# Performance work log

Hardware: AMD Instinct MI355X
Metric: run time of the kernel (lower is better)

Reference implementation:

```python
import jax, jax.numpy as jnp
import numpy as np

VIEW, SEQ, HID = 8, 2048, 1024
ATT = HID // VIEW  # 128


def setup_inputs() -> dict:
    key = jax.random.key(0)
    ks = jax.random.split(key, 12)
    std = 0.02
    return {
        "q": jax.random.normal(ks[0], (VIEW, SEQ, HID), jnp.float32),
        "k": jax.random.normal(ks[1], (VIEW, SEQ, HID), jnp.float32),
        "v": jax.random.normal(ks[2], (VIEW, SEQ, HID), jnp.float32),
        "attn_bias": jax.random.normal(ks[3], (VIEW, SEQ, SEQ), jnp.float32) * std,
        "wq": jax.random.normal(ks[4], (HID, ATT), jnp.float32) * std,
        "bq": jnp.zeros((ATT,), jnp.float32),
        "wk": jax.random.normal(ks[5], (HID, ATT), jnp.float32) * std,
        "bk": jnp.zeros((ATT,), jnp.float32),
        "wv": jax.random.normal(ks[6], (HID, ATT), jnp.float32) * std,
        "bv": jnp.zeros((ATT,), jnp.float32),
        "wo": jax.random.normal(ks[7], (VIEW * ATT, HID), jnp.float32) * std,
        "bo": jnp.zeros((HID,), jnp.float32),
    }


def reference(q, k, v, attn_bias, wq, bq, wk, bk, wv, bv, wo, bo):
    att = wq.shape[1]
    scale = att ** (-0.5)
    qh = (q @ wq + bq) * scale            # [V, S, A]
    kh = k @ wk + bk                      # [V, S, A]
    vh = v @ wv + bv                      # [V, S, A]
    scores = jnp.einsum("vqa,vka->vqk", qh, kh)   # [V, S, S]
    attn = jax.nn.softmax(scores, axis=2)
    # NOTE: source adds the bias AFTER softmax; dropout p=0 (identity).
    attn = attn + attn_bias
    x = jnp.einsum("vqk,vka->vqa", attn, vh)      # [V, S, A]
    vdim, sdim, adim = x.shape
    x = jnp.transpose(x, (1, 0, 2)).reshape(sdim, vdim * adim)  # [S, V*A]
    return x @ wo + bo                    # [S, HID]
```

## Files before the change

kernel.cpp:

```cpp
#include <hip/hip_runtime.h>
#include <math.h>

#define VIEWS 8
#define SEQ 2048
#define HID 1024
#define ATT 128
#define QSCALE 0.08838834764831845f

typedef __attribute__((ext_vector_type(8))) short short8;
typedef __attribute__((ext_vector_type(4))) float f32x4;

__device__ __forceinline__ unsigned short f2bf(float f) {
  union { float f; unsigned u; } a; a.f = f;
  unsigned r = a.u + 0x7FFF + ((a.u >> 16) & 1);
  return (unsigned short)(r >> 16);
}

__global__ __launch_bounds__(256)
void transpose_cvt_f32_bf16(const float* __restrict__ in,
                            unsigned short* __restrict__ out, int R, int C) {
  __shared__ alignas(16) unsigned short T[64][72];
  const int tid = threadIdx.x;
  const int r0 = blockIdx.y * 64, c0 = blockIdx.x * 64;
  const int tr = tid >> 2, tc = (tid & 3) * 16;
#pragma unroll
  for (int u = 0; u < 4; ++u) {
    float4 t = *(const float4*)&in[(size_t)(r0 + tr) * C + c0 + tc + u * 4];
    T[tc + u * 4 + 0][tr] = f2bf(t.x);
    T[tc + u * 4 + 1][tr] = f2bf(t.y);
    T[tc + u * 4 + 2][tr] = f2bf(t.z);
    T[tc + u * 4 + 3][tr] = f2bf(t.w);
  }
  __syncthreads();
  const int oc = tid >> 2, orr = (tid & 3) * 16;
#pragma unroll
  for (int u = 0; u < 2; ++u)
    *(short8*)&out[(size_t)(c0 + oc) * R + r0 + orr + u * 8] =
        *(const short8*)&T[oc][orr + u * 8];
}

__global__ __launch_bounds__(256)
void transpose_qkvw(const float* __restrict__ wq, const float* __restrict__ wk,
                    const float* __restrict__ wv, unsigned short* __restrict__ oq,
                    unsigned short* __restrict__ ok, unsigned short* __restrict__ ov) {
  __shared__ alignas(16) unsigned short T[64][72];
  const int z = blockIdx.z;
  const float* in = (z == 0) ? wq : (z == 1) ? wk : wv;
  unsigned short* out = (z == 0) ? oq : (z == 1) ? ok : ov;
  const int R = HID, C = ATT;
  const int tid = threadIdx.x;
  const int r0 = blockIdx.y * 64, c0 = blockIdx.x * 64;
  const int tr = tid >> 2, tc = (tid & 3) * 16;
#pragma unroll
  for (int u = 0; u < 4; ++u) {
    float4 t = *(const float4*)&in[(size_t)(r0 + tr) * C + c0 + tc + u * 4];
    T[tc + u * 4 + 0][tr] = f2bf(t.x);
    T[tc + u * 4 + 1][tr] = f2bf(t.y);
    T[tc + u * 4 + 2][tr] = f2bf(t.z);
    T[tc + u * 4 + 3][tr] = f2bf(t.w);
  }
  __syncthreads();
  const int oc = tid >> 2, orr = (tid & 3) * 16;
#pragma unroll
  for (int u = 0; u < 2; ++u)
    *(short8*)&out[(size_t)(c0 + oc) * R + r0 + orr + u * 8] =
        *(const short8*)&T[oc][orr + u * 8];
}

__global__ __launch_bounds__(256, 4)
void qkv_proj(const float* __restrict__ q, const float* __restrict__ k,
              const float* __restrict__ v, const unsigned short* __restrict__ wqT,
              const unsigned short* __restrict__ wkT,
              const unsigned short* __restrict__ wvT,
              const float* __restrict__ bq, const float* __restrict__ bk,
              const float* __restrict__ bv, unsigned short* __restrict__ qh,
              unsigned short* __restrict__ kh, unsigned short* __restrict__ vhT) {
  const int z = blockIdx.z;
  const float* A = (z == 0) ? q : (z == 1) ? k : v;
  const unsigned short* B = (z == 0) ? wqT : (z == 1) ? wkT : wvT;
  const float* bias = (z == 0) ? bq : (z == 1) ? bk : bv;
  const float scale = (z == 0) ? QSCALE : 1.0f;
  const int tid = threadIdx.x;
  const int w = tid >> 6, lane = tid & 63;
  const int l16 = lane & 15, quad = lane >> 4;
  const int mbase = blockIdx.x * 32 + (w & 1) * 16;
  const int n0 = (w >> 1) * 64;

  const float* arow = &A[(size_t)(mbase + l16) * HID + quad * 8];
  const unsigned short* bbase = &B[(size_t)(n0 + l16) * HID + quad * 8];

  f32x4 acc[4];
#pragma unroll
  for (int i = 0; i < 4; ++i) acc[i] = (f32x4)0.f;

#pragma unroll 2
  for (int k0 = 0; k0 < HID; k0 += 64) {
    const float4 a0 = *(const float4*)&arow[k0];
    const float4 a1 = *(const float4*)&arow[k0 + 4];
    const float4 a2 = *(const float4*)&arow[k0 + 32];
    const float4 a3 = *(const float4*)&arow[k0 + 36];
    short8 bfr[8];
#pragma unroll
    for (int nt = 0; nt < 4; ++nt) {
      bfr[nt * 2]     = *(const short8*)&bbase[(size_t)nt * 16 * HID + k0];
      bfr[nt * 2 + 1] = *(const short8*)&bbase[(size_t)nt * 16 * HID + k0 + 32];
    }
    short8 af0, af1;
    af0[0] = (short)f2bf(a0.x); af0[1] = (short)f2bf(a0.y);
    af0[2] = (short)f2bf(a0.z); af0[3] = (short)f2bf(a0.w);
    af0[4] = (short)f2bf(a1.x); af0[5] = (short)f2bf(a1.y);
    af0[6] = (short)f2bf(a1.z); af0[7] = (short)f2bf(a1.w);
    af1[0] = (short)f2bf(a2.x); af1[1] = (short)f2bf(a2.y);
    af1[2] = (short)f2bf(a2.z); af1[3] = (short)f2bf(a2.w);
    af1[4] = (short)f2bf(a3.x); af1[5] = (short)f2bf(a3.y);
    af1[6] = (short)f2bf(a3.z); af1[7] = (short)f2bf(a3.w);
#pragma unroll
    for (int nt = 0; nt < 4; ++nt) {
      acc[nt] = __builtin_amdgcn_mfma_f32_16x16x32_bf16(af0, bfr[nt * 2],     acc[nt], 0, 0, 0);
      acc[nt] = __builtin_amdgcn_mfma_f32_16x16x32_bf16(af1, bfr[nt * 2 + 1], acc[nt], 0, 0, 0);
    }
  }

  if (z < 2) {
    unsigned short* outp = (z == 0) ? qh : kh;
#pragma unroll
    for (int nt = 0; nt < 4; ++nt) {
      const int col = n0 + nt * 16 + l16;
      const float bvv = bias[col];
#pragma unroll
      for (int reg = 0; reg < 4; ++reg) {
        const int row = mbase + quad * 4 + reg;
        outp[(size_t)row * ATT + col] = f2bf((acc[nt][reg] + bvv) * scale);
      }
    }
  } else {
    const int gr = mbase + quad * 4;
    const int vi = gr >> 11, s = gr & (SEQ - 1);
#pragma unroll
    for (int nt = 0; nt < 4; ++nt) {
      const int col = n0 + nt * 16 + l16;
      const float bvv = bias[col];
      ushort4 pk;
      pk.x = f2bf(acc[nt][0] + bvv);
      pk.y = f2bf(acc[nt][1] + bvv);
      pk.z = f2bf(acc[nt][2] + bvv);
      pk.w = f2bf(acc[nt][3] + bvv);
      *(ushort4*)&vhT[((size_t)vi * ATT + col) * SEQ + s] = pk;
    }
  }
}

__global__ __launch_bounds__(256, 1)
void flash_fused(const unsigned short* __restrict__ qh,
                 const unsigned short* __restrict__ kh,
                 const unsigned short* __restrict__ vhT,
                 const float* __restrict__ ab,
                 unsigned short* __restrict__ xbf) {
  __shared__ alignas(16) unsigned short Qs[64][136];
  __shared__ alignas(16) unsigned short Ks[2][64][136];
  __shared__ alignas(16) unsigned short VTs[2][128][72];
  __shared__ alignas(16) unsigned short Ps[64][72];
  const int tid = threadIdx.x;
  const int vi = blockIdx.x;
  const int q0 = blockIdx.y * 64;
  const int w = tid >> 6, lane = tid & 63;
  const int l16 = lane & 15, quad = lane >> 4;
  const int wb = w * 16;

  const int kr_ = tid >> 2, kc_ = (tid & 3) * 32;
  const int vr_ = tid >> 1, vc_ = (tid & 1) * 32;
  const unsigned short* kbase = &kh[((size_t)vi * SEQ + kr_) * ATT + kc_];
  const unsigned short* vbase = &vhT[((size_t)vi * ATT + vr_) * SEQ + vc_];

  {
    const int r = tid >> 2, c = (tid & 3) * 32;
    const unsigned short* src = &qh[((size_t)vi * SEQ + q0 + r) * ATT + c];
#pragma unroll
    for (int u = 0; u < 4; ++u)
      *(short8*)&Qs[r][c + u * 8] = *(const short8*)&src[u * 8];
  }

  short8 krg[4], vrg[4];
#pragma unroll
  for (int u = 0; u < 4; ++u) krg[u] = *(const short8*)&kbase[u * 8];
#pragma unroll
  for (int u = 0; u < 4; ++u) vrg[u] = *(const short8*)&vbase[u * 8];

  __syncthreads();
  short8 aF[4];
#pragma unroll
  for (int ks = 0; ks < 4; ++ks)
    aF[ks] = *(const short8*)&Qs[wb + l16][ks * 32 + quad * 8];

  float l_r[4] = {0.f, 0.f, 0.f, 0.f};
  f32x4 o[8], o2[8];
#pragma unroll
  for (int i = 0; i < 8; ++i) { o[i] = (f32x4)0.f; o2[i] = (f32x4)0.f; }

  const float* abrow = &ab[((size_t)vi * SEQ + q0 + wb + l16) * SEQ];

  for (int t = 0; t < SEQ / 64; ++t) {
    const int kt = t * 64;
    const int cur = t & 1;
    float4 abv[4];
    abv[0] = *(const float4*)&abrow[kt + quad * 8];
    abv[1] = *(const float4*)&abrow[kt + quad * 8 + 4];
    abv[2] = *(const float4*)&abrow[kt + 32 + quad * 8];
    abv[3] = *(const float4*)&abrow[kt + 32 + quad * 8 + 4];
#pragma unroll
    for (int u = 0; u < 4; ++u)
      *(short8*)&Ks[cur][kr_][kc_ + u * 8] = krg[u];
#pragma unroll
    for (int u = 0; u < 4; ++u)
      *(short8*)&VTs[cur][vr_][vc_ + u * 8] = vrg[u];
    __syncthreads();
    if (t + 1 < SEQ / 64) {
      const unsigned short* kp = kbase + (size_t)(kt + 64) * ATT;
      const unsigned short* vp = vbase + (kt + 64);
#pragma unroll
      for (int u = 0; u < 4; ++u) krg[u] = *(const short8*)&kp[u * 8];
#pragma unroll
      for (int u = 0; u < 4; ++u) vrg[u] = *(const short8*)&vp[u * 8];
    }
    f32x4 sc[4];
#pragma unroll
    for (int i = 0; i < 4; ++i) sc[i] = (f32x4)0.f;
#pragma unroll
    for (int nt = 0; nt < 4; ++nt) {
#pragma unroll
      for (int ks = 0; ks < 4; ++ks) {
        short8 bF = *(const short8*)&Ks[cur][nt * 16 + l16][ks * 32 + quad * 8];
        sc[nt] = __builtin_amdgcn_mfma_f32_16x16x32_bf16(aF[ks], bF, sc[nt], 0, 0, 0);
      }
    }
#pragma unroll
    for (int nt = 0; nt < 4; ++nt) {
#pragma unroll
      for (int reg = 0; reg < 4; ++reg) {
        float p = __expf(sc[nt][reg]);
        l_r[reg] += p;
        Ps[wb + quad * 4 + reg][nt * 16 + l16] = f2bf(p);
      }
    }
#pragma unroll
    for (int ks = 0; ks < 2; ++ks) {
      short8 pF = *(const short8*)&Ps[wb + l16][ks * 32 + quad * 8];
      short8 bB;
      {
        const float4 u0 = abv[ks * 2], u1 = abv[ks * 2 + 1];
        bB[0] = (short)f2bf(u0.x); bB[1] = (short)f2bf(u0.y);
        bB[2] = (short)f2bf(u0.z); bB[3] = (short)f2bf(u0.w);
        bB[4] = (short)f2bf(u1.x); bB[5] = (short)f2bf(u1.y);
        bB[6] = (short)f2bf(u1.z); bB[7] = (short)f2bf(u1.w);
      }
#pragma unroll
      for (int at = 0; at < 8; ++at) {
        short8 vF = *(const short8*)&VTs[cur][at * 16 + l16][ks * 32 + quad * 8];
        o[at]  = __builtin_amdgcn_mfma_f32_16x16x32_bf16(pF, vF, o[at], 0, 0, 0);
        o2[at] = __builtin_amdgcn_mfma_f32_16x16x32_bf16(bB, vF, o2[at], 0, 0, 0);
      }
    }
  }
  float inv_l[4];
#pragma unroll
  for (int reg = 0; reg < 4; ++reg) {
    float l = l_r[reg];
    l += __shfl_xor(l, 1, 64);
    l += __shfl_xor(l, 2, 64);
    l += __shfl_xor(l, 4, 64);
    l += __shfl_xor(l, 8, 64);
    inv_l[reg] = 1.0f / l;
  }
#pragma unroll
  for (int at = 0; at < 8; ++at) {
    const int col = vi * ATT + at * 16 + l16;
#pragma unroll
    for (int reg = 0; reg < 4; ++reg) {
      const int row = q0 + wb + quad * 4 + reg;
      xbf[(size_t)row * HID + col] = f2bf(o[at][reg] * inv_l[reg] + o2[at][reg]);
    }
  }
}

__global__ __launch_bounds__(256)
void outproj_gemm(const unsigned short* __restrict__ A,
                  const unsigned short* __restrict__ B,
                  const float* __restrict__ bias, float* __restrict__ out) {
  __shared__ alignas(16) unsigned short As[2][64][72];
  __shared__ alignas(16) unsigned short Bs[2][128][72];
  const int tid = threadIdx.x;
  const int m0 = blockIdx.x * 64;
  const int n0 = blockIdx.y * 128;
  const int w = tid >> 6, lane = tid & 63;
  const int l16 = lane & 15, quad = lane >> 4;
  const int ar = tid >> 2, ac = (tid & 3) * 16;
  const int br = tid >> 1, bc = (tid & 1) * 32;
  const unsigned short* abase = &A[(size_t)(m0 + ar) * HID + ac];
  const unsigned short* bbase = &B[(size_t)(n0 + br) * HID + bc];

  f32x4 acc[8];
#pragma unroll
  for (int i = 0; i < 8; ++i) acc[i] = (f32x4)0.f;

  short8 arg0, arg1, brg[4];
  arg0 = *(const short8*)&abase[0];
  arg1 = *(const short8*)&abase[8];
#pragma unroll
  for (int u = 0; u < 4; ++u) brg[u] = *(const short8*)&bbase[u * 8];

  for (int kk = 0; kk < HID / 64; ++kk) {
    const int cur = kk & 1;
    *(short8*)&As[cur][ar][ac]     = arg0;
    *(short8*)&As[cur][ar][ac + 8] = arg1;
#pragma unroll
    for (int u = 0; u < 4; ++u)
      *(short8*)&Bs[cur][br][bc + u * 8] = brg[u];
    __syncthreads();
    if (kk + 1 < HID / 64) {
      const unsigned short* ap = abase + (kk + 1) * 64;
      const unsigned short* bp = bbase + (kk + 1) * 64;
      arg0 = *(const short8*)&ap[0];
      arg1 = *(const short8*)&ap[8];
#pragma unroll
      for (int u = 0; u < 4; ++u) brg[u] = *(const short8*)&bp[u * 8];
    }
#pragma unroll
    for (int ks = 0; ks < 2; ++ks) {
      short8 af = *(const short8*)&As[cur][w * 16 + l16][ks * 32 + quad * 8];
#pragma unroll
      for (int nt = 0; nt < 8; ++nt) {
        short8 bf = *(const short8*)&Bs[cur][nt * 16 + l16][ks * 32 + quad * 8];
        acc[nt] = __builtin_amdgcn_mfma_f32_16x16x32_bf16(af, bf, acc[nt], 0, 0, 0);
      }
    }
  }
#pragma unroll
  for (int nt = 0; nt < 8; ++nt) {
    const int col = n0 + nt * 16 + l16;
    const float bvv = bias[col];
#pragma unroll
    for (int reg = 0; reg < 4; ++reg) {
      const int row = m0 + w * 16 + quad * 4 + reg;
      out[(size_t)row * HID + col] = acc[nt][reg] + bvv;
    }
  }
}

extern "C" void kernel_launch(void* const* d_in, const int* in_sizes, int n_in,
                              void* d_out, int out_size, void* d_ws, size_t ws_size,
                              hipStream_t stream) {
  const float* q   = (const float*)d_in[0];
  const float* k   = (const float*)d_in[1];
  const float* v   = (const float*)d_in[2];
  const float* ab  = (const float*)d_in[3];
  const float* wq  = (const float*)d_in[4];
  const float* bq  = (const float*)d_in[5];
  const float* wk  = (const float*)d_in[6];
  const float* bk  = (const float*)d_in[7];
  const float* wv  = (const float*)d_in[8];
  const float* bv  = (const float*)d_in[9];
  const float* wo  = (const float*)d_in[10];
  const float* bo  = (const float*)d_in[11];
  float* out = (float*)d_out;

  char* ws = (char*)d_ws;
  const size_t PROJ_B = (size_t)VIEWS * SEQ * ATT * 2;
  unsigned short* qh  = (unsigned short*)(ws);
  unsigned short* kh  = (unsigned short*)(ws + PROJ_B);
  unsigned short* vhT = (unsigned short*)(ws + 2 * PROJ_B);
  unsigned short* xbf = (unsigned short*)(ws + 3 * PROJ_B);
  char* wbase = ws + 4 * PROJ_B;
  unsigned short* wqT = (unsigned short*)(wbase);
  unsigned short* wkT = (unsigned short*)(wbase + 262144);
  unsigned short* wvT = (unsigned short*)(wbase + 2 * 262144);
  unsigned short* woT = (unsigned short*)(wbase + 3 * 262144);

  dim3 blk(256);
  transpose_qkvw<<<dim3(2, 16, 3), blk, 0, stream>>>(wq, wk, wv, wqT, wkT, wvT);
  transpose_cvt_f32_bf16<<<dim3(16, 16), blk, 0, stream>>>(wo, woT, HID, HID);
  qkv_proj<<<dim3(512, 1, 3), blk, 0, stream>>>(q, k, v, wqT, wkT, wvT,
                                                bq, bk, bv, qh, kh, vhT);
  flash_fused<<<dim3(VIEWS, SEQ / 64), blk, 0, stream>>>(qh, kh, vhT, ab, xbf);
  outproj_gemm<<<dim3(SEQ / 64, HID / 128), blk, 0, stream>>>(xbf, woT, bo, out);
}
```

Baseline: 486.0 us.

## Stage QKV projection operands via LDS async loads and halve flash query tile

```diff
diff --git a/kernel.cpp b/kernel.cpp
--- a/kernel.cpp
+++ b/kernel.cpp
@@ -9,6 +9,11 @@
 
 typedef __attribute__((ext_vector_type(8))) short short8;
 typedef __attribute__((ext_vector_type(4))) float f32x4;
+
+#define GLOAD_LDS16(g, l)                                                     \
+  __builtin_amdgcn_global_load_lds(                                           \
+      (const __attribute__((address_space(1))) unsigned int*)(g),             \
+      (__attribute__((address_space(3))) unsigned int*)(l), 16, 0, 0)
 
 __device__ __forceinline__ unsigned short f2bf(float f) {
   union { float f; unsigned u; } a; a.f = f;
@@ -67,7 +72,7 @@
         *(const short8*)&T[oc][orr + u * 8];
 }
 
-__global__ __launch_bounds__(256, 4)
+__global__ __launch_bounds__(256, 2)
 void qkv_proj(const float* __restrict__ q, const float* __restrict__ k,
               const float* __restrict__ v, const unsigned short* __restrict__ wqT,
               const unsigned short* __restrict__ wkT,
@@ -75,6 +80,8 @@
               const float* __restrict__ bq, const float* __restrict__ bk,
               const float* __restrict__ bv, unsigned short* __restrict__ qh,
               unsigned short* __restrict__ kh, unsigned short* __restrict__ vhT) {
+  __shared__ alignas(16) float Af[2][32][64];
+  __shared__ alignas(16) unsigned short Bf[2][128][64];
   const int z = blockIdx.z;
   const float* A = (z == 0) ? q : (z == 1) ? k : v;
   const unsigned short* B = (z == 0) ? wqT : (z == 1) ? wkT : wvT;
@@ -83,28 +90,40 @@
   const int tid = threadIdx.x;
   const int w = tid >> 6, lane = tid & 63;
   const int l16 = lane & 15, quad = lane >> 4;
-  const int mbase = blockIdx.x * 32 + (w & 1) * 16;
+  const int m0 = blockIdx.x * 32;
+  const int wm = (w & 1) * 16;
   const int n0 = (w >> 1) * 64;
 
-  const float* arow = &A[(size_t)(mbase + l16) * HID + quad * 8];
-  const unsigned short* bbase = &B[(size_t)(n0 + l16) * HID + quad * 8];
+  const float* ag[2];
+#pragma unroll
+  for (int j = 0; j < 2; ++j)
+    ag[j] = &A[(size_t)(m0 + (w * 2 + j) * 4 + (lane >> 4)) * HID + (lane & 15) * 4];
+  const unsigned short* bg[4];
+#pragma unroll
+  for (int j = 0; j < 4; ++j)
+    bg[j] = &B[(size_t)((w * 4 + j) * 8 + (lane >> 3)) * HID + (lane & 7) * 8];
 
   f32x4 acc[4];
 #pragma unroll
   for (int i = 0; i < 4; ++i) acc[i] = (f32x4)0.f;
 
-#pragma unroll 2
-  for (int k0 = 0; k0 < HID; k0 += 64) {
-    const float4 a0 = *(const float4*)&arow[k0];
-    const float4 a1 = *(const float4*)&arow[k0 + 4];
-    const float4 a2 = *(const float4*)&arow[k0 + 32];
-    const float4 a3 = *(const float4*)&arow[k0 + 36];
-    short8 bfr[8];
-#pragma unroll
-    for (int nt = 0; nt < 4; ++nt) {
-      bfr[nt * 2]     = *(const short8*)&bbase[(size_t)nt * 16 * HID + k0];
-      bfr[nt * 2 + 1] = *(const short8*)&bbase[(size_t)nt * 16 * HID + k0 + 32];
-    }
+#define QKV_STAGE(nxt, k0)                                                    \
+  do {                                                                        \
+    _Pragma("unroll") for (int j = 0; j < 2; ++j)                             \
+        GLOAD_LDS16(ag[j] + (k0), &Af[nxt][(w * 2 + j) * 4][0]);              \
+    _Pragma("unroll") for (int j = 0; j < 4; ++j)                             \
+        GLOAD_LDS16(bg[j] + (k0), &Bf[nxt][(w * 4 + j) * 8][0]);              \
+  } while (0)
+
+  QKV_STAGE(0, 0);
+  int cur = 0;
+  for (int kk = 0; kk < HID / 64; ++kk) {
+    __syncthreads();
+    if (kk + 1 < HID / 64) QKV_STAGE(cur ^ 1, (kk + 1) * 64);
+    const float4 a0 = *(const float4*)&Af[cur][wm + l16][quad * 8];
+    const float4 a1 = *(const float4*)&Af[cur][wm + l16][quad * 8 + 4];
+    const float4 a2 = *(const float4*)&Af[cur][wm + l16][32 + quad * 8];
+    const float4 a3 = *(const float4*)&Af[cur][wm + l16][36 + quad * 8];
     short8 af0, af1;
     af0[0] = (short)f2bf(a0.x); af0[1] = (short)f2bf(a0.y);
     af0[2] = (short)f2bf(a0.z); af0[3] = (short)f2bf(a0.w);
@@ -116,10 +135,14 @@
     af1[6] = (short)f2bf(a3.z); af1[7] = (short)f2bf(a3.w);
 #pragma unroll
     for (int nt = 0; nt < 4; ++nt) {
-      acc[nt] = __builtin_amdgcn_mfma_f32_16x16x32_bf16(af0, bfr[nt * 2],     acc[nt], 0, 0, 0);
-      acc[nt] = __builtin_amdgcn_mfma_f32_16x16x32_bf16(af1, bfr[nt * 2 + 1], acc[nt], 0, 0, 0);
-    }
-  }
+      const short8 b0 = *(const short8*)&Bf[cur][n0 + nt * 16 + l16][quad * 8];
+      const short8 b1 = *(const short8*)&Bf[cur][n0 + nt * 16 + l16][32 + quad * 8];
+      acc[nt] = __builtin_amdgcn_mfma_f32_16x16x32_bf16(af0, b0, acc[nt], 0, 0, 0);
+      acc[nt] = __builtin_amdgcn_mfma_f32_16x16x32_bf16(af1, b1, acc[nt], 0, 0, 0);
+    }
+    cur ^= 1;
+  }
+#undef QKV_STAGE
 
   if (z < 2) {
     unsigned short* outp = (z == 0) ? qh : kh;
@@ -129,12 +152,12 @@
       const float bvv = bias[col];
 #pragma unroll
       for (int reg = 0; reg < 4; ++reg) {
-        const int row = mbase + quad * 4 + reg;
+        const int row = m0 + wm + quad * 4 + reg;
         outp[(size_t)row * ATT + col] = f2bf((acc[nt][reg] + bvv) * scale);
       }
     }
   } else {
-    const int gr = mbase + quad * 4;
+    const int gr = m0 + wm + quad * 4;
     const int vi = gr >> 11, s = gr & (SEQ - 1);
 #pragma unroll
     for (int nt = 0; nt < 4; ++nt) {
@@ -150,22 +173,25 @@
   }
 }
 
-__global__ __launch_bounds__(256, 1)
+__global__ __launch_bounds__(256, 2)
 void flash_fused(const unsigned short* __restrict__ qh,
                  const unsigned short* __restrict__ kh,
                  const unsigned short* __restrict__ vhT,
                  const float* __restrict__ ab,
                  unsigned short* __restrict__ xbf) {
-  __shared__ alignas(16) unsigned short Qs[64][136];
+  __shared__ alignas(16) char QPs[32 * 136 * 2];
   __shared__ alignas(16) unsigned short Ks[2][64][136];
   __shared__ alignas(16) unsigned short VTs[2][128][72];
-  __shared__ alignas(16) unsigned short Ps[64][72];
+  unsigned short (*Qs)[136] = (unsigned short(*)[136])QPs;
+  unsigned short (*Ps)[72]  = (unsigned short(*)[72])QPs;
+  float* Ls = (float*)(QPs + 32 * 72 * 2);
   const int tid = threadIdx.x;
   const int vi = blockIdx.x;
-  const int q0 = blockIdx.y * 64;
+  const int q0 = blockIdx.y * 32;
   const int w = tid >> 6, lane = tid & 63;
   const int l16 = lane & 15, quad = lane >> 4;
-  const int wb = w * 16;
+  const int wq_ = (w & 1) * 16;
+  const int wh = w >> 1;
 
   const int kr_ = tid >> 2, kc_ = (tid & 3) * 32;
   const int vr_ = tid >> 1, vc_ = (tid & 1) * 32;
@@ -173,13 +199,11 @@
   const unsigned short* vbase = &vhT[((size_t)vi * ATT + vr_) * SEQ + vc_];
 
   {
-    const int r = tid >> 2, c = (tid & 3) * 32;
+    const int r = tid >> 3, c = (tid & 7) * 16;
     const unsigned short* src = &qh[((size_t)vi * SEQ + q0 + r) * ATT + c];
-#pragma unroll
-    for (int u = 0; u < 4; ++u)
-      *(short8*)&Qs[r][c + u * 8] = *(const short8*)&src[u * 8];
-  }
-
+    *(short8*)&Qs[r][c]     = *(const short8*)&src[0];
+    *(short8*)&Qs[r][c + 8] = *(const short8*)&src[8];
+  }
   short8 krg[4], vrg[4];
 #pragma unroll
   for (int u = 0; u < 4; ++u) krg[u] = *(const short8*)&kbase[u * 8];
@@ -190,14 +214,14 @@
   short8 aF[4];
 #pragma unroll
   for (int ks = 0; ks < 4; ++ks)
-    aF[ks] = *(const short8*)&Qs[wb + l16][ks * 32 + quad * 8];
+    aF[ks] = *(const short8*)&Qs[wq_ + l16][ks * 32 + quad * 8];
 
   float l_r[4] = {0.f, 0.f, 0.f, 0.f};
-  f32x4 o[8], o2[8];
-#pragma unroll
-  for (int i = 0; i < 8; ++i) { o[i] = (f32x4)0.f; o2[i] = (f32x4)0.f; }
-
-  const float* abrow = &ab[((size_t)vi * SEQ + q0 + wb + l16) * SEQ];
+  f32x4 o[4], o2[4];
+#pragma unroll
+  for (int i = 0; i < 4; ++i) { o[i] = (f32x4)0.f; o2[i] = (f32x4)0.f; }
+
+  const float* abrow = &ab[((size_t)vi * SEQ + q0 + wq_ + l16) * SEQ];
 
   for (int t = 0; t < SEQ / 64; ++t) {
     const int kt = t * 64;
@@ -222,29 +246,29 @@
 #pragma unroll
       for (int u = 0; u < 4; ++u) vrg[u] = *(const short8*)&vp[u * 8];
     }
-    f32x4 sc[4];
-#pragma unroll
-    for (int i = 0; i < 4; ++i) sc[i] = (f32x4)0.f;
-#pragma unroll
-    for (int nt = 0; nt < 4; ++nt) {
+    f32x4 sc[2];
+    sc[0] = (f32x4)0.f; sc[1] = (f32x4)0.f;
+#pragma unroll
+    for (int nt = 0; nt < 2; ++nt) {
 #pragma unroll
       for (int ks = 0; ks < 4; ++ks) {
-        short8 bF = *(const short8*)&Ks[cur][nt * 16 + l16][ks * 32 + quad * 8];
+        const short8 bF = *(const short8*)&Ks[cur][wh * 32 + nt * 16 + l16][ks * 32 + quad * 8];
         sc[nt] = __builtin_amdgcn_mfma_f32_16x16x32_bf16(aF[ks], bF, sc[nt], 0, 0, 0);
       }
     }
 #pragma unroll
-    for (int nt = 0; nt < 4; ++nt) {
+    for (int nt = 0; nt < 2; ++nt) {
 #pragma unroll
       for (int reg = 0; reg < 4; ++reg) {
-        float p = __expf(sc[nt][reg]);
+        const float p = __expf(sc[nt][reg]);
         l_r[reg] += p;
-        Ps[wb + quad * 4 + reg][nt * 16 + l16] = f2bf(p);
-      }
-    }
+        Ps[wq_ + quad * 4 + reg][wh * 32 + nt * 16 + l16] = f2bf(p);
+      }
+    }
+    __syncthreads();
 #pragma unroll
     for (int ks = 0; ks < 2; ++ks) {
-      short8 pF = *(const short8*)&Ps[wb + l16][ks * 32 + quad * 8];
+      const short8 pF = *(const short8*)&Ps[wq_ + l16][ks * 32 + quad * 8];
       short8 bB;
       {
         const float4 u0 = abv[ks * 2], u1 = abv[ks * 2 + 1];
@@ -254,14 +278,13 @@
         bB[6] = (short)f2bf(u1.z); bB[7] = (short)f2bf(u1.w);
       }
 #pragma unroll
-      for (int at = 0; at < 8; ++at) {
-        short8 vF = *(const short8*)&VTs[cur][at * 16 + l16][ks * 32 + quad * 8];
+      for (int at = 0; at < 4; ++at) {
+        const short8 vF = *(const short8*)&VTs[cur][wh * 64 + at * 16 + l16][ks * 32 + quad * 8];
         o[at]  = __builtin_amdgcn_mfma_f32_16x16x32_bf16(pF, vF, o[at], 0, 0, 0);
         o2[at] = __builtin_amdgcn_mfma_f32_16x16x32_bf16(bB, vF, o2[at], 0, 0, 0);
       }
     }
   }
-  float inv_l[4];
 #pragma unroll
   for (int reg = 0; reg < 4; ++reg) {
     float l = l_r[reg];
@@ -269,14 +292,26 @@
     l += __shfl_xor(l, 2, 64);
     l += __shfl_xor(l, 4, 64);
     l += __shfl_xor(l, 8, 64);
-    inv_l[reg] = 1.0f / l;
-  }
-#pragma unroll
-  for (int at = 0; at < 8; ++at) {
-    const int col = vi * ATT + at * 16 + l16;
+    l_r[reg] = l;
+  }
+  if (l16 == 0) {
+#pragma unroll
+    for (int reg = 0; reg < 4; ++reg)
+      Ls[wh * 32 + wq_ + quad * 4 + reg] = l_r[reg];
+  }
+  __syncthreads();
+  float inv_l[4];
+#pragma unroll
+  for (int reg = 0; reg < 4; ++reg) {
+    const int row = wq_ + quad * 4 + reg;
+    inv_l[reg] = 1.0f / (Ls[row] + Ls[32 + row]);
+  }
+#pragma unroll
+  for (int at = 0; at < 4; ++at) {
+    const int col = vi * ATT + wh * 64 + at * 16 + l16;
 #pragma unroll
     for (int reg = 0; reg < 4; ++reg) {
-      const int row = q0 + wb + quad * 4 + reg;
+      const int row = q0 + wq_ + quad * 4 + reg;
       xbf[(size_t)row * HID + col] = f2bf(o[at][reg] * inv_l[reg] + o2[at][reg]);
     }
   }
@@ -380,6 +415,6 @@
   transpose_cvt_f32_bf16<<<dim3(16, 16), blk, 0, stream>>>(wo, woT, HID, HID);
   qkv_proj<<<dim3(512, 1, 3), blk, 0, stream>>>(q, k, v, wqT, wkT, wvT,
                                                 bq, bk, bv, qh, kh, vhT);
-  flash_fused<<<dim3(VIEWS, SEQ / 64), blk, 0, stream>>>(qh, kh, vhT, ab, xbf);
+  flash_fused<<<dim3(VIEWS, SEQ / 32), blk, 0, stream>>>(qh, kh, vhT, ab, xbf);
   outproj_gemm<<<dim3(SEQ / 64, HID / 128), blk, 0, stream>>>(xbf, woT, bo, out);
 }
```

New measurement: 427.7 us. 1.14x faster.

## Stage QKV projection tiles through LDS with async global_load_lds double buffering

Applied to the files above, without the earlier changes.

```diff
diff --git a/kernel.cpp b/kernel.cpp
--- a/kernel.cpp
+++ b/kernel.cpp
@@ -9,6 +9,11 @@
 
 typedef __attribute__((ext_vector_type(8))) short short8;
 typedef __attribute__((ext_vector_type(4))) float f32x4;
+
+#define GLOAD_LDS16(g, l)                                                     \
+  __builtin_amdgcn_global_load_lds(                                           \
+      (const __attribute__((address_space(1))) unsigned int*)(g),             \
+      (__attribute__((address_space(3))) unsigned int*)(l), 16, 0, 0)
 
 __device__ __forceinline__ unsigned short f2bf(float f) {
   union { float f; unsigned u; } a; a.f = f;
@@ -67,7 +72,7 @@
         *(const short8*)&T[oc][orr + u * 8];
 }
 
-__global__ __launch_bounds__(256, 4)
+__global__ __launch_bounds__(256, 2)
 void qkv_proj(const float* __restrict__ q, const float* __restrict__ k,
               const float* __restrict__ v, const unsigned short* __restrict__ wqT,
               const unsigned short* __restrict__ wkT,
@@ -75,6 +80,8 @@
               const float* __restrict__ bq, const float* __restrict__ bk,
               const float* __restrict__ bv, unsigned short* __restrict__ qh,
               unsigned short* __restrict__ kh, unsigned short* __restrict__ vhT) {
+  __shared__ alignas(16) float Af[2][32][64];
+  __shared__ alignas(16) unsigned short Bf[2][128][64];
   const int z = blockIdx.z;
   const float* A = (z == 0) ? q : (z == 1) ? k : v;
   const unsigned short* B = (z == 0) ? wqT : (z == 1) ? wkT : wvT;
@@ -83,28 +90,49 @@
   const int tid = threadIdx.x;
   const int w = tid >> 6, lane = tid & 63;
   const int l16 = lane & 15, quad = lane >> 4;
-  const int mbase = blockIdx.x * 32 + (w & 1) * 16;
+  const int m0 = blockIdx.x * 32;
+  const int wm = (w & 1) * 16;
   const int n0 = (w >> 1) * 64;
 
-  const float* arow = &A[(size_t)(mbase + l16) * HID + quad * 8];
-  const unsigned short* bbase = &B[(size_t)(n0 + l16) * HID + quad * 8];
+  const float* ag[2];
+#pragma unroll
+  for (int j = 0; j < 2; ++j) {
+    const int c = w * 2 + j;
+    const int r = c * 4 + (lane >> 4);
+    const int sg = (lane & 15) ^ (r & 7);
+    ag[j] = &A[(size_t)(m0 + r) * HID + sg * 4];
+  }
+  const unsigned short* bg[4];
+#pragma unroll
+  for (int j = 0; j < 4; ++j) {
+    const int c = w * 4 + j;
+    const int r = c * 8 + (lane >> 3);
+    const int sg = (lane & 7) ^ (r & 7);
+    bg[j] = &B[(size_t)r * HID + sg * 8];
+  }
 
   f32x4 acc[4];
 #pragma unroll
   for (int i = 0; i < 4; ++i) acc[i] = (f32x4)0.f;
 
-#pragma unroll 2
-  for (int k0 = 0; k0 < HID; k0 += 64) {
-    const float4 a0 = *(const float4*)&arow[k0];
-    const float4 a1 = *(const float4*)&arow[k0 + 4];
-    const float4 a2 = *(const float4*)&arow[k0 + 32];
-    const float4 a3 = *(const float4*)&arow[k0 + 36];
-    short8 bfr[8];
-#pragma unroll
-    for (int nt = 0; nt < 4; ++nt) {
-      bfr[nt * 2]     = *(const short8*)&bbase[(size_t)nt * 16 * HID + k0];
-      bfr[nt * 2 + 1] = *(const short8*)&bbase[(size_t)nt * 16 * HID + k0 + 32];
-    }
+#define QKV_STAGE(nxt, k0)                                                    \
+  do {                                                                        \
+    _Pragma("unroll") for (int j = 0; j < 2; ++j)                             \
+        GLOAD_LDS16(ag[j] + (k0), &Af[nxt][(w * 2 + j) * 4][0]);              \
+    _Pragma("unroll") for (int j = 0; j < 4; ++j)                             \
+        GLOAD_LDS16(bg[j] + (k0), &Bf[nxt][(w * 4 + j) * 8][0]);              \
+  } while (0)
+
+  QKV_STAGE(0, 0);
+  int cur = 0;
+  const int akey = l16 & 7;
+  for (int kk = 0; kk < HID / 64; ++kk) {
+    __syncthreads();
+    if (kk + 1 < HID / 64) QKV_STAGE(cur ^ 1, (kk + 1) * 64);
+    const float4 a0 = *(const float4*)&Af[cur][wm + l16][((quad * 2)     ^ akey) * 4];
+    const float4 a1 = *(const float4*)&Af[cur][wm + l16][((quad * 2 + 1) ^ akey) * 4];
+    const float4 a2 = *(const float4*)&Af[cur][wm + l16][((quad * 2 + 8) ^ akey) * 4];
+    const float4 a3 = *(const float4*)&Af[cur][wm + l16][((quad * 2 + 9) ^ akey) * 4];
     short8 af0, af1;
     af0[0] = (short)f2bf(a0.x); af0[1] = (short)f2bf(a0.y);
     af0[2] = (short)f2bf(a0.z); af0[3] = (short)f2bf(a0.w);
@@ -116,10 +144,15 @@
     af1[6] = (short)f2bf(a3.z); af1[7] = (short)f2bf(a3.w);
 #pragma unroll
     for (int nt = 0; nt < 4; ++nt) {
-      acc[nt] = __builtin_amdgcn_mfma_f32_16x16x32_bf16(af0, bfr[nt * 2],     acc[nt], 0, 0, 0);
-      acc[nt] = __builtin_amdgcn_mfma_f32_16x16x32_bf16(af1, bfr[nt * 2 + 1], acc[nt], 0, 0, 0);
-    }
-  }
+      const int brow = n0 + nt * 16 + l16;
+      const short8 b0 = *(const short8*)&Bf[cur][brow][((quad)     ^ akey) * 8];
+      const short8 b1 = *(const short8*)&Bf[cur][brow][((quad + 4) ^ akey) * 8];
+      acc[nt] = __builtin_amdgcn_mfma_f32_16x16x32_bf16(af0, b0, acc[nt], 0, 0, 0);
+      acc[nt] = __builtin_amdgcn_mfma_f32_16x16x32_bf16(af1, b1, acc[nt], 0, 0, 0);
+    }
+    cur ^= 1;
+  }
+#undef QKV_STAGE
 
   if (z < 2) {
     unsigned short* outp = (z == 0) ? qh : kh;
@@ -129,12 +162,12 @@
       const float bvv = bias[col];
 #pragma unroll
       for (int reg = 0; reg < 4; ++reg) {
-        const int row = mbase + quad * 4 + reg;
+        const int row = m0 + wm + quad * 4 + reg;
         outp[(size_t)row * ATT + col] = f2bf((acc[nt][reg] + bvv) * scale);
       }
     }
   } else {
-    const int gr = mbase + quad * 4;
+    const int gr = m0 + wm + quad * 4;
     const int vi = gr >> 11, s = gr & (SEQ - 1);
 #pragma unroll
     for (int nt = 0; nt < 4; ++nt) {
```

New measurement: 412.0 us. 1.18x faster.
